# Performance work log

Hardware: AMD Instinct MI355X
Metric: run time of the kernel (lower is better)

The kernel has to match this reference:

```python
import jax, jax.numpy as jnp
import numpy as np

N_NODES = 50000
IN_CH = 512
OUT_CH = 512
N_EDGES = 800000


def setup_inputs() -> dict:
    key = jax.random.key(0)
    k_x, k_e, k_w, k_b = jax.random.split(key, 4)
    x = jax.random.normal(k_x, (N_NODES, IN_CH), dtype=jnp.float32)
    edge_index = jax.random.randint(k_e, (2, N_EDGES), 0, N_NODES, dtype=jnp.int32)
    # nn.Linear(in_channels*2, out_channels): weight (out, 2*in), bias (out,)
    bound = 1.0 / np.sqrt(2 * IN_CH)
    W = jax.random.uniform(k_w, (OUT_CH, 2 * IN_CH), minval=-bound, maxval=bound, dtype=jnp.float32)
    b = jax.random.uniform(k_b, (OUT_CH,), minval=-bound, maxval=bound, dtype=jnp.float32)
    return {"x": x, "edge_index": edge_index, "W": W, "b": b}


def reference(x, edge_index, W, b):
    # SAGE(v) = W . concat(h_v, mean_{u in N(v)} h_u) + b
    src, dst = edge_index[0], edge_index[1]
    src_feats = x[src]                                        # (E, C) gather
    neighbor_sum = jax.ops.segment_sum(src_feats, dst, num_segments=x.shape[0])  # (N, C)
    neighbor_count = jax.ops.segment_sum(
        jnp.ones((src.shape[0],), dtype=x.dtype), dst, num_segments=x.shape[0]
    )                                                          # (N,)
    neighbor_count = jnp.maximum(neighbor_count, 1.0)
    neighbor_mean = neighbor_sum / neighbor_count[:, None]
    h = jnp.concatenate([x, neighbor_mean], axis=-1)           # (N, 2C)
    return h @ W.T + b                                         # (N, out)
```

## Files before the change

kernel.cpp:

```cpp
#include <hip/hip_runtime.h>
#include <stdint.h>

#define CI 512
#define CO 512
#define CPAD 8

typedef __attribute__((ext_vector_type(4))) float f32x4;
typedef __attribute__((ext_vector_type(8))) __bf16 bf16x8;

#define AS1 __attribute__((address_space(1)))
#define AS3 __attribute__((address_space(3)))

__device__ __forceinline__ unsigned short f2bf_bits(float f) {
  union { float f; unsigned int u; } v; v.f = f;
  unsigned int u = v.u;
  unsigned int lsb = (u >> 16) & 1u;
  u += 0x7fffu + lsb;
  return (unsigned short)(u >> 16);
}

__global__ void k_prep0(const int* __restrict__ dst, int* __restrict__ cnt, int E,
                        const float* __restrict__ W, unsigned short* __restrict__ Wb,
                        int nw4, int bd) {
  const int b = blockIdx.x;
  if (b < bd) {
    int e = b * 256 + threadIdx.x;
    if (e < E) atomicAdd(&cnt[dst[e] * CPAD], 1);
  } else {
    int i = (b - bd) * 256 + threadIdx.x;
    if (i < nw4) {
      float4 v = reinterpret_cast<const float4*>(W)[i];
      ushort4 o;
      o.x = f2bf_bits(v.x); o.y = f2bf_bits(v.y);
      o.z = f2bf_bits(v.z); o.w = f2bf_bits(v.w);
      reinterpret_cast<ushort4*>(Wb)[i] = o;
    }
  }
}

__global__ void k_bsum(const int* __restrict__ cnt, int* __restrict__ bsum, int n) {
  int t = threadIdx.x;
  int i = blockIdx.x * 256 + t;
  int v = (i < n) ? cnt[(size_t)i * CPAD] : 0;
  #pragma unroll
  for (int off = 32; off; off >>= 1) v += __shfl_down(v, off, 64);
  __shared__ int ws[4];
  if ((t & 63) == 0) ws[t >> 6] = v;
  __syncthreads();
  if (t == 0) bsum[blockIdx.x] = ws[0] + ws[1] + ws[2] + ws[3];
}

__global__ void k_scanf(const int* __restrict__ cnt, const int* __restrict__ bsum,
                        int* __restrict__ rowptr, int n, int nb) {
  int t = threadIdx.x, lane = t & 63, w = t >> 6;
  __shared__ int ws1[4], ws2[4], sboff;

  int v0 = (t < nb) ? bsum[t] : 0;
  int s0 = v0;
  #pragma unroll
  for (int off = 1; off < 64; off <<= 1) {
    int u = __shfl_up(s0, off, 64);
    if (lane >= off) s0 += u;
  }
  if (lane == 63) ws1[w] = s0;
  __syncthreads();
  if (t == blockIdx.x) {
    int add0 = 0;
    for (int j = 0; j < w; ++j) add0 += ws1[j];
    sboff = s0 + add0 - v0;
  }
  __syncthreads();

  int i = blockIdx.x * 256 + t;
  int v = (i < n) ? cnt[(size_t)i * CPAD] : 0;
  int s = v;
  #pragma unroll
  for (int off = 1; off < 64; off <<= 1) {
    int u = __shfl_up(s, off, 64);
    if (lane >= off) s += u;
  }
  if (lane == 63) ws2[w] = s;
  __syncthreads();
  int add = sboff;
  for (int j = 0; j < w; ++j) add += ws2[j];
  if (i < n) rowptr[i + 1] = s + add;
  if (i == 0) rowptr[0] = 0;
}

__global__ void k_fillx(const int* __restrict__ src, const int* __restrict__ dst,
                        const int* __restrict__ rowptr,
                        int* __restrict__ curA, int* __restrict__ curB,
                        unsigned short* __restrict__ csr, int E, int half,
                        const float* __restrict__ x, unsigned short* __restrict__ xb,
                        int nx4, int bf) {
  const int b = blockIdx.x;
  if (b < bf) {
    int e = b * 256 + threadIdx.x;
    if (e < E) {
      int d = dst[e];
      int s = src[e];
      if (s < half) {
        int pos = atomicAdd(&curA[(size_t)d * CPAD], 1);
        csr[rowptr[d] + pos] = (unsigned short)s;
      } else {
        int pos = atomicAdd(&curB[(size_t)d * CPAD], 1);
        csr[rowptr[d + 1] - 1 - pos] = (unsigned short)s;
      }
    }
  } else {
    int i = (b - bf) * 256 + threadIdx.x;
    if (i < nx4) {
      f32x4 v = __builtin_nontemporal_load(reinterpret_cast<const f32x4*>(x) + i);
      ushort4 o;
      o.x = f2bf_bits(v.x); o.y = f2bf_bits(v.y);
      o.z = f2bf_bits(v.z); o.w = f2bf_bits(v.w);
      reinterpret_cast<ushort4*>(xb)[i] = o;
    }
  }
}

__device__ __forceinline__ void acc8(float* s, uint4 r) {
  const unsigned int u[4] = {r.x, r.y, r.z, r.w};
  #pragma unroll
  for (int k = 0; k < 4; ++k) {
    union { unsigned int u; float f; } lo, hi;
    lo.u = u[k] << 16;
    hi.u = u[k] & 0xffff0000u;
    s[2 * k]     += lo.f;
    s[2 * k + 1] += hi.f;
  }
}

__global__ __launch_bounds__(256) void k_aggregate(
    const unsigned short* __restrict__ xb,
    const int* __restrict__ rowptr,
    const unsigned short* __restrict__ csr,
    unsigned short* __restrict__ meanS, int Nn) {
  const int s  = blockIdx.x & 7;
  const int nb = blockIdx.x >> 3;
  const int wv = threadIdx.x >> 6;
  const int lane = threadIdx.x & 63;
  const int g = lane >> 3, li = lane & 7;
  const int node = nb * 32 + wv * 8 + g;

  int beg = 0, deg = 0;
  if (node < Nn) {
    beg = rowptr[node];
    deg = rowptr[node + 1] - beg;
  }
  float acc[8] = {};
  const unsigned short* __restrict__ xs = xb + s * 64 + li * 8;

  int j = 0;
  for (; j + 4 <= deg; j += 4) {
    int i0 = (int)csr[beg + j];
    int i1 = (int)csr[beg + j + 1];
    int i2 = (int)csr[beg + j + 2];
    int i3 = (int)csr[beg + j + 3];
    uint4 r0 = *reinterpret_cast<const uint4*>(xs + (size_t)i0 * CI);
    uint4 r1 = *reinterpret_cast<const uint4*>(xs + (size_t)i1 * CI);
    uint4 r2 = *reinterpret_cast<const uint4*>(xs + (size_t)i2 * CI);
    uint4 r3 = *reinterpret_cast<const uint4*>(xs + (size_t)i3 * CI);
    acc8(acc, r0);
    acc8(acc, r1);
    acc8(acc, r2);
    acc8(acc, r3);
  }
  for (; j < deg; ++j) {
    int i0 = (int)csr[beg + j];
    uint4 r0 = *reinterpret_cast<const uint4*>(xs + (size_t)i0 * CI);
    acc8(acc, r0);
  }

  if (node < Nn) {
    const float inv = 1.f / fmaxf((float)deg, 1.f);
    unsigned short ob[8];
    #pragma unroll
    for (int k = 0; k < 8; ++k) ob[k] = f2bf_bits(acc[k] * inv);
    uint4 w;
    w.x = (unsigned int)ob[0] | ((unsigned int)ob[1] << 16);
    w.y = (unsigned int)ob[2] | ((unsigned int)ob[3] << 16);
    w.z = (unsigned int)ob[4] | ((unsigned int)ob[5] << 16);
    w.w = (unsigned int)ob[6] | ((unsigned int)ob[7] << 16);
    *reinterpret_cast<uint4*>(meanS + ((size_t)s * Nn + node) * 64 + li * 8) = w;
  }
}

#define BM 128
#define BN 128
#define BK 64
#define SLOT_SH 16384
#define BOFF 8192
#define EPAD 132

#define WAITV(N) asm volatile("s_waitcnt vmcnt(" #N ")" ::: "memory")

__global__ __launch_bounds__(256) void k_gemm(
    const unsigned short* __restrict__ xb,
    const unsigned short* __restrict__ meanS,
    const unsigned short* __restrict__ Wb,
    const float* __restrict__ bias,
    float* __restrict__ out, int M) {
  __shared__ unsigned short lds[2 * SLOT_SH];
  const int tid = threadIdx.x;
  const int ntn = CO / BN;

  const int nwg = gridDim.x;
  const int q = nwg >> 3, r = nwg & 7;
  const int xcd = blockIdx.x & 7, lid = blockIdx.x >> 3;
  const int wg = (xcd < r ? xcd * (q + 1) : r * (q + 1) + (xcd - r) * q) + lid;

  const int tm = wg / ntn, tn = wg % ntn;
  const int m0 = tm * BM, n0 = tn * BN;
  const int lane = tid & 63, wvid = tid >> 6;
  const int wm = wvid >> 1, wn = wvid & 1;
  const int lrow = lane & 15;

  int arow[4], gra[4], scol8[4];
  #pragma unroll
  for (int i = 0; i < 4; ++i) {
    int idx = i * 256 + tid;
    int rr = idx >> 3;
    arow[i] = rr;
    scol8[i] = ((idx & 7) ^ (rr & 7)) * 8;
    int g = m0 + rr;
    gra[i] = g < M ? g : M - 1;
  }

  const size_t Nn64 = (size_t)M * 64;

  f32x4 acc[4][4] = {};

  auto stage = [&](int kt, int sl) {
    unsigned short* sa = &lds[sl * SLOT_SH];
    unsigned short* sb = sa + BOFF;
    if (kt < 8) {
      const int ka = kt * 64;
      #pragma unroll
      for (int i = 0; i < 4; ++i)
        __builtin_amdgcn_global_load_lds(
          (const AS1 unsigned int*)(uintptr_t)(xb + (size_t)gra[i] * CI + ka + scol8[i]),
          (AS3 unsigned int*)(uintptr_t)(&sa[(size_t)(i * 256 + tid) * 8]), 16, 0, 0);
    } else {
      const unsigned short* __restrict__ A = meanS + (size_t)(kt - 8) * Nn64;
      #pragma unroll
      for (int i = 0; i < 4; ++i)
        __builtin_amdgcn_global_load_lds(
          (const AS1 unsigned int*)(uintptr_t)(A + (size_t)gra[i] * 64 + scol8[i]),
          (AS3 unsigned int*)(uintptr_t)(&sa[(size_t)(i * 256 + tid) * 8]), 16, 0, 0);
    }
    const int kw = kt * 64;
    #pragma unroll
    for (int i = 0; i < 4; ++i)
      __builtin_amdgcn_global_load_lds(
        (const AS1 unsigned int*)(uintptr_t)(Wb + (size_t)(n0 + arow[i]) * (2 * CI) + kw + scol8[i]),
        (AS3 unsigned int*)(uintptr_t)(&sb[(size_t)(i * 256 + tid) * 8]), 16, 0, 0);
  };

  auto compute = [&](int sl) {
    const unsigned short* __restrict__ La = &lds[sl * SLOT_SH];
    const unsigned short* __restrict__ Lb = La + BOFF;
    #pragma unroll
    for (int kk = 0; kk < 2; ++kk) {
      const int crd = kk * 4 + (lane >> 4);
      bf16x8 af[4], bf[4];
      #pragma unroll
      for (int mi = 0; mi < 4; ++mi) {
        const int rr = wm * 64 + mi * 16 + lrow;
        af[mi] = *reinterpret_cast<const bf16x8*>(&La[rr * BK + ((crd ^ (rr & 7)) * 8)]);
      }
      #pragma unroll
      for (int ni = 0; ni < 4; ++ni) {
        const int rb = wn * 64 + ni * 16 + lrow;
        bf[ni] = *reinterpret_cast<const bf16x8*>(&Lb[rb * BK + ((crd ^ (rb & 7)) * 8)]);
      }
      __builtin_amdgcn_s_setprio(1);
      #pragma unroll
      for (int mi = 0; mi < 4; ++mi)
        #pragma unroll
        for (int ni = 0; ni < 4; ++ni)
          acc[mi][ni] = __builtin_amdgcn_mfma_f32_16x16x32_bf16(af[mi], bf[ni], acc[mi][ni], 0, 0, 0);
      __builtin_amdgcn_s_setprio(0);
    }
  };

  stage(0, 0);

  #pragma unroll
  for (int t = 0; t < 16; ++t) {
    if (t < 15) {
      stage(t + 1, (t + 1) & 1);
      WAITV(8);
    } else {
      WAITV(0);
    }
    __builtin_amdgcn_s_barrier();
    __builtin_amdgcn_sched_barrier(0);
    compute(t & 1);
    __builtin_amdgcn_sched_barrier(0);
    __builtin_amdgcn_s_barrier();
  }

  __syncthreads();
  float* lds_c = reinterpret_cast<float*>(&lds[0]);
  const int lj = lane >> 4;
  float bv[4];
  #pragma unroll
  for (int ni = 0; ni < 4; ++ni) bv[ni] = bias[n0 + wn * 64 + ni * 16 + lrow];

  #pragma unroll
  for (int cw = 0; cw < 2; ++cw) {
    #pragma unroll
    for (int mi = 0; mi < 4; ++mi) {
      if (wm == cw) {
        #pragma unroll
        for (int ni = 0; ni < 4; ++ni)
          #pragma unroll
          for (int j = 0; j < 4; ++j)
            lds_c[(lj * 4 + j) * EPAD + wn * 64 + ni * 16 + lrow] = acc[mi][ni][j] + bv[ni];
      }
      __syncthreads();
      #pragma unroll
      for (int p = 0; p < 2; ++p) {
        int linear = p * 256 + tid;
        int rl = linear >> 5;
        int c4 = (linear & 31) << 2;
        int row = m0 + cw * 64 + mi * 16 + rl;
        if (row < M) {
          f32x4 v = *reinterpret_cast<const f32x4*>(&lds_c[rl * EPAD + c4]);
          __builtin_nontemporal_store(v,
            reinterpret_cast<f32x4*>(&out[(size_t)row * CO + n0 + c4]));
        }
      }
      __syncthreads();
    }
  }
}

extern "C" void kernel_launch(void* const* d_in, const int* in_sizes, int n_in,
                              void* d_out, int out_size, void* d_ws, size_t ws_size,
                              hipStream_t stream) {
  (void)n_in; (void)out_size; (void)ws_size;
  const float* x    = (const float*)d_in[0];
  const int*   ei   = (const int*)d_in[1];
  const float* W    = (const float*)d_in[2];
  const float* bias = (const float*)d_in[3];
  float* out = (float*)d_out;

  const int Nn = in_sizes[0] / CI;
  const int E  = in_sizes[1] / 2;
  const int* src = ei;
  const int* dst = ei + E;

  const int nblk = (Nn + 255) / 256;

  int* cnt    = (int*)d_ws;
  int* curA   = cnt + (size_t)Nn * CPAD;
  int* curB   = curA + (size_t)Nn * CPAD;
  int* rowptr = curB + (size_t)Nn * CPAD;
  int* bsum   = rowptr + (Nn + 1);
  uintptr_t p = (uintptr_t)(bsum + nblk);
  p = (p + 255) & ~(uintptr_t)255;
  unsigned short* csr = (unsigned short*)p;
  p = (uintptr_t)(csr + E);
  p = (p + 255) & ~(uintptr_t)255;
  unsigned short* xb    = (unsigned short*)p;
  unsigned short* meanS = xb + (size_t)Nn * CI;
  unsigned short* Wb    = meanS + (size_t)Nn * CI;

  hipMemsetAsync(cnt, 0, (size_t)3 * Nn * CPAD * sizeof(int), stream);

  const int nx4 = (Nn * CI) / 4;
  const int nw4 = (CO * 2 * CI) / 4;
  const int bx = (nx4 + 255) / 256;
  const int bw = (nw4 + 255) / 256;
  const int be = (E + 255) / 256;

  k_prep0<<<be + bw, 256, 0, stream>>>(dst, cnt, E, W, Wb, nw4, be);
  k_bsum<<<nblk, 256, 0, stream>>>(cnt, bsum, Nn);
  k_scanf<<<nblk, 256, 0, stream>>>(cnt, bsum, rowptr, Nn, nblk);
  k_fillx<<<be + bx, 256, 0, stream>>>(src, dst, rowptr, curA, curB, csr, E, Nn / 2,
                                       x, xb, nx4, be);

  const int nab = ((Nn + 31) / 32) * 8;
  k_aggregate<<<nab, 256, 0, stream>>>(xb, rowptr, csr, meanS, Nn);

  const int mtiles = (Nn + BM - 1) / BM;
  k_gemm<<<mtiles * (CO / BN), 256, 0, stream>>>(xb, meanS, Wb, bias, out, Nn);
}
```

Before: 246.3 us.

## Load GEMM A operand directly to registers and deepen B LDS pipeline

The GEMM now loads the A tiles (x and mean features) straight from global memory into registers, double-buffered across iterations, and keeps only the W tile in LDS with a 4-slot ring prefetched three stages ahead. Separately, zeroing of the curA/curB cursors moves from a large memset into the scan kernel, shrinking the memset. The aim is to cut LDS traffic and round trips for A and to hide global latency better, at the cost of more registers and unswizzled per-lane global reads for A.

New measurement: 306.6 us. 1.24x slower.

```diff
diff --git a/kernel.cpp b/kernel.cpp
--- a/kernel.cpp
+++ b/kernel.cpp
@@ -51,7 +51,9 @@
 }
 
 __global__ void k_scanf(const int* __restrict__ cnt, const int* __restrict__ bsum,
-                        int* __restrict__ rowptr, int n, int nb) {
+                        int* __restrict__ rowptr,
+                        int* __restrict__ curA, int* __restrict__ curB,
+                        int n, int nb) {
   int t = threadIdx.x, lane = t & 63, w = t >> 6;
   __shared__ int ws1[4], ws2[4], sboff;
 
@@ -83,7 +85,11 @@
   __syncthreads();
   int add = sboff;
   for (int j = 0; j < w; ++j) add += ws2[j];
-  if (i < n) rowptr[i + 1] = s + add;
+  if (i < n) {
+    rowptr[i + 1] = s + add;
+    curA[(size_t)i * CPAD] = 0;
+    curB[(size_t)i * CPAD] = 0;
+  }
   if (i == 0) rowptr[0] = 0;
 }
 
@@ -189,8 +195,7 @@
 #define BM 128
 #define BN 128
 #define BK 64
-#define SLOT_SH 16384
-#define BOFF 8192
+#define SLOT_SH 8192
 #define EPAD 132
 
 #define WAITV(N) asm volatile("s_waitcnt vmcnt(" #N ")" ::: "memory")
@@ -201,7 +206,7 @@
     const unsigned short* __restrict__ Wb,
     const float* __restrict__ bias,
     float* __restrict__ out, int M) {
-  __shared__ unsigned short lds[2 * SLOT_SH];
+  __shared__ unsigned short lds[4 * SLOT_SH];
   const int tid = threadIdx.x;
   const int ntn = CO / BN;
 
@@ -215,60 +220,59 @@
   const int lane = tid & 63, wvid = tid >> 6;
   const int wm = wvid >> 1, wn = wvid & 1;
   const int lrow = lane & 15;
-
-  int arow[4], gra[4], scol8[4];
+  const int lj4 = lane >> 4;
+
+  int brow[4], bcol8[4];
   #pragma unroll
   for (int i = 0; i < 4; ++i) {
     int idx = i * 256 + tid;
     int rr = idx >> 3;
-    arow[i] = rr;
-    scol8[i] = ((idx & 7) ^ (rr & 7)) * 8;
-    int g = m0 + rr;
-    gra[i] = g < M ? g : M - 1;
+    brow[i] = rr;
+    bcol8[i] = ((idx & 7) ^ (rr & 7)) * 8;
+  }
+
+  int garow[4];
+  #pragma unroll
+  for (int mi = 0; mi < 4; ++mi) {
+    int g = m0 + wm * 64 + mi * 16 + lrow;
+    garow[mi] = g < M ? g : M - 1;
   }
 
   const size_t Nn64 = (size_t)M * 64;
 
   f32x4 acc[4][4] = {};
-
-  auto stage = [&](int kt, int sl) {
-    unsigned short* sa = &lds[sl * SLOT_SH];
-    unsigned short* sb = sa + BOFF;
-    if (kt < 8) {
-      const int ka = kt * 64;
-      #pragma unroll
-      for (int i = 0; i < 4; ++i)
-        __builtin_amdgcn_global_load_lds(
-          (const AS1 unsigned int*)(uintptr_t)(xb + (size_t)gra[i] * CI + ka + scol8[i]),
-          (AS3 unsigned int*)(uintptr_t)(&sa[(size_t)(i * 256 + tid) * 8]), 16, 0, 0);
-    } else {
-      const unsigned short* __restrict__ A = meanS + (size_t)(kt - 8) * Nn64;
-      #pragma unroll
-      for (int i = 0; i < 4; ++i)
-        __builtin_amdgcn_global_load_lds(
-          (const AS1 unsigned int*)(uintptr_t)(A + (size_t)gra[i] * 64 + scol8[i]),
-          (AS3 unsigned int*)(uintptr_t)(&sa[(size_t)(i * 256 + tid) * 8]), 16, 0, 0);
-    }
+  bf16x8 afbuf[2][8];
+
+  auto stageB = [&](int kt, int sl) {
+    unsigned short* sb = &lds[sl * SLOT_SH];
     const int kw = kt * 64;
     #pragma unroll
     for (int i = 0; i < 4; ++i)
       __builtin_amdgcn_global_load_lds(
-        (const AS1 unsigned int*)(uintptr_t)(Wb + (size_t)(n0 + arow[i]) * (2 * CI) + kw + scol8[i]),
+        (const AS1 unsigned int*)(uintptr_t)(Wb + (size_t)(n0 + brow[i]) * (2 * CI) + kw + bcol8[i]),
         (AS3 unsigned int*)(uintptr_t)(&sb[(size_t)(i * 256 + tid) * 8]), 16, 0, 0);
   };
 
-  auto compute = [&](int sl) {
-    const unsigned short* __restrict__ La = &lds[sl * SLOT_SH];
-    const unsigned short* __restrict__ Lb = La + BOFF;
+  auto loadA = [&](int kt, bf16x8* dst) {
     #pragma unroll
     for (int kk = 0; kk < 2; ++kk) {
-      const int crd = kk * 4 + (lane >> 4);
-      bf16x8 af[4], bf[4];
+      const int crd = kk * 4 + lj4;
       #pragma unroll
       for (int mi = 0; mi < 4; ++mi) {
-        const int rr = wm * 64 + mi * 16 + lrow;
-        af[mi] = *reinterpret_cast<const bf16x8*>(&La[rr * BK + ((crd ^ (rr & 7)) * 8)]);
-      }
+        const unsigned short* p;
+        if (kt < 8) p = xb + (size_t)garow[mi] * CI + kt * 64 + crd * 8;
+        else        p = meanS + (size_t)(kt - 8) * Nn64 + (size_t)garow[mi] * 64 + crd * 8;
+        dst[kk * 4 + mi] = *reinterpret_cast<const bf16x8*>(p);
+      }
+    }
+  };
+
+  auto compute = [&](int sl, const bf16x8* af) {
+    const unsigned short* __restrict__ Lb = &lds[sl * SLOT_SH];
+    #pragma unroll
+    for (int kk = 0; kk < 2; ++kk) {
+      const int crd = kk * 4 + lj4;
+      bf16x8 bf[4];
       #pragma unroll
       for (int ni = 0; ni < 4; ++ni) {
         const int rb = wn * 64 + ni * 16 + lrow;
@@ -279,24 +283,28 @@
       for (int mi = 0; mi < 4; ++mi)
         #pragma unroll
         for (int ni = 0; ni < 4; ++ni)
-          acc[mi][ni] = __builtin_amdgcn_mfma_f32_16x16x32_bf16(af[mi], bf[ni], acc[mi][ni], 0, 0, 0);
+          acc[mi][ni] = __builtin_amdgcn_mfma_f32_16x16x32_bf16(af[kk * 4 + mi], bf[ni], acc[mi][ni], 0, 0, 0);
       __builtin_amdgcn_s_setprio(0);
     }
   };
 
-  stage(0, 0);
+  stageB(0, 0);
+  stageB(1, 1);
+  stageB(2, 2);
+  loadA(0, afbuf[0]);
 
   #pragma unroll
   for (int t = 0; t < 16; ++t) {
-    if (t < 15) {
-      stage(t + 1, (t + 1) & 1);
-      WAITV(8);
-    } else {
-      WAITV(0);
-    }
+    if (t < 15) loadA(t + 1, afbuf[(t + 1) & 1]);
+    if (t < 13) stageB(t + 3, (t + 3) & 3);
+    if (t == 0)       WAITV(12);
+    else if (t < 13)  WAITV(16);
+    else if (t == 13) WAITV(12);
+    else if (t == 14) WAITV(8);
+    else              WAITV(0);
     __builtin_amdgcn_s_barrier();
     __builtin_amdgcn_sched_barrier(0);
-    compute(t & 1);
+    compute(t & 3, afbuf[t & 1]);
     __builtin_amdgcn_sched_barrier(0);
     __builtin_amdgcn_s_barrier();
   }
@@ -368,7 +376,7 @@
   unsigned short* meanS = xb + (size_t)Nn * CI;
   unsigned short* Wb    = meanS + (size_t)Nn * CI;
 
-  hipMemsetAsync(cnt, 0, (size_t)3 * Nn * CPAD * sizeof(int), stream);
+  hipMemsetAsync(cnt, 0, (size_t)Nn * CPAD * sizeof(int), stream);
 
   const int nx4 = (Nn * CI) / 4;
   const int nw4 = (CO * 2 * CI) / 4;
@@ -378,7 +386,7 @@
 
   k_prep0<<<be + bw, 256, 0, stream>>>(dst, cnt, E, W, Wb, nw4, be);
   k_bsum<<<nblk, 256, 0, stream>>>(cnt, bsum, Nn);
-  k_scanf<<<nblk, 256, 0, stream>>>(cnt, bsum, rowptr, Nn, nblk);
+  k_scanf<<<nblk, 256, 0, stream>>>(cnt, bsum, rowptr, curA, curB, Nn, nblk);
   k_fillx<<<be + bx, 256, 0, stream>>>(src, dst, rowptr, curA, curB, csr, E, Nn / 2,
                                        x, xb, nx4, be);
 
```
